# Optimization experiments

Hardware: AMD Instinct MI355X
Metric: run time of the kernel (lower is better)

Reference implementation:

```python
import jax, jax.numpy as jnp
import numpy as np

NMS_THRESH = 0.3  # default nms_thresh in DetNet.predict


def setup_inputs() -> dict:
    key = jax.random.key(0)
    k1, k2, k3, k4 = jax.random.split(key, 4)
    W, N = 8, 1024
    det = jax.random.uniform(k1, (W, N, 5), dtype=jnp.float32)          # (conf, cx, cy, w, h) in [0,1)
    offsets = jax.random.uniform(k2, (W, 5), dtype=jnp.float32) * 0.5   # window offset vector (0, left, top, 0, 0)-like
    scales = jax.random.uniform(k3, (W, 5), dtype=jnp.float32) * 0.5 + 0.25  # window scale vector
    b = jax.random.uniform(k4, (W, 4), dtype=jnp.float32)
    # (valid_left, valid_right, valid_top, valid_bottom) with left<right, top<bottom
    bounds = jnp.stack([0.3 * b[:, 0], 0.7 + 0.3 * b[:, 1],
                        0.3 * b[:, 2], 0.7 + 0.3 * b[:, 3]], axis=-1)
    return {"det": det, "offsets": offsets, "scales": scales, "bounds": bounds}


def _pairwise_iou(boxes):
    # boxes: [M,4] in (x1,y1,x2,y2)
    x1, y1, x2, y2 = boxes[:, 0], boxes[:, 1], boxes[:, 2], boxes[:, 3]
    area = jnp.clip(x2 - x1, 0.0) * jnp.clip(y2 - y1, 0.0)              # [M]
    iw = jnp.clip(jnp.minimum(x2[:, None], x2[None, :]) - jnp.maximum(x1[:, None], x1[None, :]), 0.0)
    ih = jnp.clip(jnp.minimum(y2[:, None], y2[None, :]) - jnp.maximum(y1[:, None], y1[None, :]), 0.0)
    inter = iw * ih                                                     # [M,M]
    union = area[:, None] + area[None, :] - inter
    return inter / jnp.maximum(union, 1e-9)


def reference(det, offsets, scales, bounds):
    W, N, _ = det.shape
    M = W * N
    cx, cy = det[..., 1], det[..., 2]                                    # [W,N]
    left, right = bounds[:, 0:1], bounds[:, 1:2]
    top, bottom = bounds[:, 2:3], bounds[:, 3:4]
    valid = (cx < right) & (cx > left) & (cy < bottom) & (cy > top)      # [W,N] border mask
    # torch.addcmul(offset, d, scale) = offset + d * scale
    d = (offsets[:, None, :] + det * scales[:, None, :]).reshape(M, 5)
    valid = valid.reshape(M)
    scores = jnp.where(valid, d[:, 0], -1.0)                             # invalid boxes never kept
    order = jnp.argsort(-scores)                                         # descending confidence
    d_s = d[order]                                                       # [M,5]
    s_s = scores[order]
    # point_form: (cx,cy,w,h) -> (x1,y1,x2,y2)
    cxy, wh = d_s[:, 1:3], d_s[:, 3:5]
    boxes = jnp.concatenate([cxy - wh * 0.5, cxy + wh * 0.5], axis=-1)
    iou = jax.lax.stop_gradient(_pairwise_iou(boxes))                    # [M,M], suppression is non-diff
    s_c = jax.lax.stop_gradient(s_s)
    idx = jnp.arange(M)

    def body(i, keep):
        # suppressed if any kept higher-score box overlaps > thresh
        sup = jnp.any(keep & (idx < i) & (iou[:, i] > NMS_THRESH))
        return keep.at[i].set(jnp.logical_and(~sup, s_c[i] > 0.0))

    keep = jax.lax.fori_loop(0, M, body, jnp.ones((M,), dtype=bool))
    return d_s * keep[:, None].astype(d_s.dtype)                         # [M,5], suppressed rows zeroed
```

## Files before the change

### kernel.cpp

```cpp
#include <hip/hip_runtime.h>
#include <cstdint>


#define M_TOT 8192
#define NMS_T 0.3f

#define WS_BOX   65536
#define WS_D     196608
#define WS_VCNT  360448
#define WS_ZROW  393216
#define WS_MASK  524288

typedef unsigned long long u64t;

__device__ __forceinline__ uint32_t desc_key(float sv) {
    uint32_t u = __float_as_uint(sv);
    uint32_t m = (u & 0x80000000u) ? ~u : (u | 0x80000000u);
    return ~m;
}

__device__ __forceinline__ u64t rdl64(u64t v, int sl) {
    unsigned lo = (unsigned)__builtin_amdgcn_readlane((int)(unsigned)v, sl);
    unsigned hi = (unsigned)__builtin_amdgcn_readlane((int)(unsigned)(v >> 32), sl);
    return ((u64t)hi << 32) | lo;
}
__device__ __forceinline__ u64t rdfl64(u64t v) {
    unsigned lo = (unsigned)__builtin_amdgcn_readfirstlane((int)(unsigned)v);
    unsigned hi = (unsigned)__builtin_amdgcn_readfirstlane((int)(unsigned)(v >> 32));
    return ((u64t)hi << 32) | lo;
}

__device__ __forceinline__ int scatter_one(
    int i, int rank, u64t key,
    const float* __restrict__ det, const float* __restrict__ offsets,
    const float* __restrict__ scales,
    float4* __restrict__ boxes_srt, float* __restrict__ d_srt)
{
    uint32_t dkey = (uint32_t)(key >> 16);
    if (dkey >= 0x7FFFFFFFu) return 0;
    int g = i >> 10;
    float d0 = __fadd_rn(offsets[g*5+0], __fmul_rn(det[i*5+0], scales[g*5+0]));
    float d1 = __fadd_rn(offsets[g*5+1], __fmul_rn(det[i*5+1], scales[g*5+1]));
    float d2 = __fadd_rn(offsets[g*5+2], __fmul_rn(det[i*5+2], scales[g*5+2]));
    float d3 = __fadd_rn(offsets[g*5+3], __fmul_rn(det[i*5+3], scales[g*5+3]));
    float d4 = __fadd_rn(offsets[g*5+4], __fmul_rn(det[i*5+4], scales[g*5+4]));
    d_srt[rank*5+0] = d0; d_srt[rank*5+1] = d1; d_srt[rank*5+2] = d2;
    d_srt[rank*5+3] = d3; d_srt[rank*5+4] = d4;
    float hw = __fmul_rn(d3, 0.5f), hh = __fmul_rn(d4, 0.5f);
    boxes_srt[rank] = make_float4(__fsub_rn(d1, hw), __fsub_rn(d2, hh),
                                  __fadd_rn(d1, hw), __fadd_rn(d2, hh));
    return 1;
}

__global__ __launch_bounds__(256) void k2_rank(
    const float* __restrict__ det, const float* __restrict__ offsets,
    const float* __restrict__ scales, const float* __restrict__ bounds,
    float4* __restrict__ boxes_srt, float* __restrict__ d_srt,
    unsigned int* __restrict__ vcnt, u64t* __restrict__ zrow,
    float* __restrict__ out)
{
    __shared__ u64t skey[M_TOT];
    __shared__ float soff[40], sscl[40], sbnd[32];
    __shared__ int sTop;
    int t = threadIdx.x;
    int lane = t & 63;
    if (t == 0) sTop = 0;
    if (t < 40) { soff[t] = offsets[t]; sscl[t] = scales[t]; }
    if (t < 32) { sbnd[t] = bounds[t]; }
    if (blockIdx.x == 0 && t < 128) zrow[t] = 0ull;
    __syncthreads();

    #pragma unroll 4
    for (int s = 0; s < 32; ++s) {
        int u = s * 256 + t;
        int g = u >> 10;
        float raw_s = det[u * 5 + 0];
        float cx    = det[u * 5 + 1];
        float cy    = det[u * 5 + 2];
        float score = __fadd_rn(soff[g * 5 + 0], __fmul_rn(raw_s, sscl[g * 5 + 0]));
        bool valid = (cx < sbnd[g*4+1]) && (cx > sbnd[g*4+0]) &&
                     (cy < sbnd[g*4+3]) && (cy > sbnd[g*4+2]);
        float sv = valid ? score : -1.0f;
        uint32_t dk = desc_key(sv);
        bool push = dk < 0x7FFFFFFFu;
        u64t key = ((u64t)dk << 16) | (unsigned)u;
        u64t bal = __ballot(push);
        if (bal) {
            int lw = 0;
            if (lane == 0) lw = atomicAdd(&sTop, __popcll(bal));
            int wbase = __builtin_amdgcn_readfirstlane(lw);
            if (push) {
                int off = __popcll(bal & ((1ull << lane) - 1ull));
                skey[wbase + off] = key;
            }
        }
    }
    __syncthreads();
    int V = sTop;
    int Vpad = (V + 15) & ~15;
    if (t < Vpad - V) skey[V + t] = ~0ull;
    {
        int zb = blockIdx.x * 160;
        for (int z = zb + t; z < zb + 160; z += 256) out[z] = 0.0f;
    }
    __syncthreads();
    if (t == 0) *vcnt = (unsigned)V;

    int grp = t >> 3;
    int jq  = t & 7;
    int i = blockIdx.x * 32 + grp;
    int g = i >> 10;
    float raw_s = det[i * 5 + 0];
    float cx    = det[i * 5 + 1];
    float cy    = det[i * 5 + 2];
    float score = __fadd_rn(soff[g * 5 + 0], __fmul_rn(raw_s, sscl[g * 5 + 0]));
    bool valid = (cx < sbnd[g*4+1]) && (cx > sbnd[g*4+0]) &&
                 (cy < sbnd[g*4+3]) && (cy > sbnd[g*4+2]);
    float sv = valid ? score : -1.0f;
    uint32_t dk = desc_key(sv);
    u64t ki = ((u64t)dk << 16) | (unsigned)i;
    const ulonglong2* skey2 = (const ulonglong2*)skey;
    int c = 0;
    int nit = Vpad >> 4;
    #pragma unroll 4
    for (int it = 0; it < nit; ++it) {
        ulonglong2 kj = skey2[it * 8 + jq];
        c += (kj.x < ki) + (kj.y < ki);
    }
    c += __shfl_xor(c, 1);
    c += __shfl_xor(c, 2);
    c += __shfl_xor(c, 4);
    if (jq == 0)
        scatter_one(i, c, ki, det, offsets, scales, boxes_srt, d_srt);
}

__global__ __launch_bounds__(256) void k_mask(
    const float4* __restrict__ boxes_srt,
    const unsigned int* __restrict__ vcnt,
    u64t* __restrict__ mask)
{
    __shared__ float4 sb[16 * 65];
    __shared__ float  sa[16 * 65];
    int V = (int)*vcnt;
    int bx = blockIdx.x, by = blockIdx.y;
    if (bx * 32 >= V) return;
    if (by * 1024 >= V) return;
    if (by * 16 + 15 < (bx * 32) >> 6) return;
    int nc = (V + 63) >> 6;
    int tid = threadIdx.x;
    int cbase = by * 1024;
    for (int u = tid; u < 1024; u += 256) {
        float4 b = boxes_srt[cbase + u];
        int c = u >> 6, jj = u & 63;
        sb[c * 65 + jj] = b;
        sa[c * 65 + jj] = __fmul_rn(fmaxf(__fsub_rn(b.z, b.x), 0.0f),
                                    fmaxf(__fsub_rn(b.w, b.y), 0.0f));
    }
    __syncthreads();
    int r = bx * 32 + (tid >> 3);
    if (r >= V) return;
    float4 bi = boxes_srt[r];
    float ai = __fmul_rn(fmaxf(__fsub_rn(bi.z, bi.x), 0.0f),
                         fmaxf(__fsub_rn(bi.w, bi.y), 0.0f));
    int rw = r >> 6;
    #pragma unroll
    for (int k = 0; k < 2; ++k) {
        int wl = (tid & 7) + k * 8;
        int w = by * 16 + wl;
        if (w < rw || w >= nc) continue;
        u64t bits = 0;
        #pragma unroll 4
        for (int jj = 0; jj < 64; ++jj) {
            float4 bj = sb[wl * 65 + jj];
            float aj = sa[wl * 65 + jj];
            float iw = fmaxf(__fsub_rn(fminf(bi.z, bj.z), fmaxf(bi.x, bj.x)), 0.0f);
            float ih = fmaxf(__fsub_rn(fminf(bi.w, bj.w), fmaxf(bi.y, bj.y)), 0.0f);
            float inter = __fmul_rn(iw, ih);
            float uni   = __fsub_rn(__fadd_rn(ai, aj), inter);
            float iou   = __fdiv_rn(inter, fmaxf(uni, 1e-9f));
            int j = w * 64 + jj;
            if (j > r && iou > NMS_T) bits |= 1ull << jj;
        }
        mask[(size_t)r * 128 + w] = bits;
    }
}

struct WSlot { ulonglong2 dl, dh, n1l, n1h, n2l, n2h; };

__device__ __forceinline__ void fill_words(
    const u64t* __restrict__ mask, int lane, int T, WSlot& w)
{
    int rl = min(T * 128 + lane,      M_TOT - 1);
    int rh = min(T * 128 + 64 + lane, M_TOT - 1);
    const ulonglong2* mrl = (const ulonglong2*)(mask + (size_t)rl * 128);
    const ulonglong2* mrh = (const ulonglong2*)(mask + (size_t)rh * 128);
    int p0 = min(T,     63);
    int p1 = min(T + 1, 63);
    int p2 = min(T + 2, 63);
    w.dl  = mrl[p0]; w.dh  = mrh[p0];
    w.n1l = mrl[p1]; w.n1h = mrh[p1];
    w.n2l = mrl[p2]; w.n2h = mrh[p2];
}

__device__ __forceinline__ void res_step(
    const u64t* __restrict__ mask,
    u64t* sdead, u64t* ck, volatile int* res_prog, volatile int* h_prog,
    int lane, int nc, int T,
    u64t& cA_lo, u64t& cA_hi, u64t& cB_lo, u64t& cB_hi, WSlot& w)
{
    if (T >= 3) {
        int need = T - 2;
        while (true) {
            int hp = (lane < 7) ? h_prog[lane] : 0x7FFFFFFF;
            if (__ballot(hp < need) == 0ull) break;
        }
    }
    u64t dlo = rdfl64(((volatile u64t*)sdead)[2 * T]);
    u64t dhi = rdfl64(((volatile u64t*)sdead)[2 * T + 1]);
    u64t live_lo = ~(dlo | cA_lo);
    u64t live_hi = ~(dhi | cA_hi);
    u64t km_lo = 0, km_hi = 0;
    while (live_lo) {
        int bs = (int)__builtin_ctzll(live_lo);
        km_lo |= 1ull << bs;
        u64t rml = rdl64(w.dl.x, bs);
        u64t rmh = rdl64(w.dl.y, bs);
        live_lo &= ~rml & ~(1ull << bs);
        live_hi &= ~rmh;
    }
    while (live_hi) {
        int bs = (int)__builtin_ctzll(live_hi);
        km_hi |= 1ull << bs;
        u64t rmh = rdl64(w.dh.y, bs);
        live_hi &= ~rmh & ~(1ull << bs);
    }
    if (lane == 0) { ck[2 * T] = km_lo; ck[2 * T + 1] = km_hi; }
    __threadfence_block();
    if (lane == 0) *res_prog = T + 1;
    u64t c1l = 0, c1h = 0, c2l = 0, c2h = 0;
    u64t km = km_lo;
    while (km) {
        int b = (int)__builtin_ctzll(km); km &= km - 1;
        c1l |= rdl64(w.n1l.x, b); c1h |= rdl64(w.n1l.y, b);
        c2l |= rdl64(w.n2l.x, b); c2h |= rdl64(w.n2l.y, b);
    }
    km = km_hi;
    while (km) {
        int b = (int)__builtin_ctzll(km); km &= km - 1;
        c1l |= rdl64(w.n1h.x, b); c1h |= rdl64(w.n1h.y, b);
        c2l |= rdl64(w.n2h.x, b); c2h |= rdl64(w.n2h.y, b);
    }
    cA_lo = cB_lo | c1l; cA_hi = cB_hi | c1h;
    cB_lo = c2l;         cB_hi = c2h;
    fill_words(mask, lane, T + 3, w);
}

__global__ __launch_bounds__(512) void k3_serial(
    const u64t* __restrict__ mask, const u64t* __restrict__ zrow,
    const float* __restrict__ d_srt, const unsigned int* __restrict__ vcnt,
    float* __restrict__ out)
{
    __shared__ u64t sdead[128];
    __shared__ u64t ck[128];
    __shared__ int  res_prog;
    __shared__ int  h_prog[7];
    int tid = threadIdx.x, wv = tid >> 6, lane = tid & 63;
    int V = (int)*vcnt;
    int nc = (V + 127) >> 7;
    if (tid < 128) {
        int bw = tid * 64;
        u64t w0 = 0;
        if (bw >= V)           w0 = ~0ull;
        else if (bw + 64 > V)  w0 = (~0ull) << (V - bw);
        sdead[tid] = w0;
        ck[tid] = 0ull;
    }
    if (tid == 0) res_prog = 0;
    if (tid < 7)  h_prog[tid] = tid;
    __syncthreads();

    if (wv == 0) {
        u64t cA_lo = 0, cA_hi = 0, cB_lo = 0, cB_hi = 0;
        WSlot WA, WB, WC;
        fill_words(mask, lane, 0, WA);
        fill_words(mask, lane, 1, WB);
        fill_words(mask, lane, 2, WC);
        for (int t = 0; t < nc; t += 3) {
            res_step(mask, sdead, ck, &res_prog, h_prog, lane, nc, t,
                     cA_lo, cA_hi, cB_lo, cB_hi, WA);
            if (t + 1 < nc)
                res_step(mask, sdead, ck, &res_prog, h_prog, lane, nc, t + 1,
                         cA_lo, cA_hi, cB_lo, cB_hi, WB);
            if (t + 2 < nc)
                res_step(mask, sdead, ck, &res_prog, h_prog, lane, nc, t + 2,
                         cA_lo, cA_hi, cB_lo, cB_hi, WC);
        }
    } else {
        int hh = wv - 1;
        for (int c = hh; c < nc; c += 7) {
            while (*(volatile int*)&res_prog <= c) __builtin_amdgcn_s_sleep(1);
            u64t kl = ((volatile u64t*)ck)[2 * c];
            u64t kh = ((volatile u64t*)ck)[2 * c + 1];
            if (kl | kh) {
                int base = c * 128;
                u64t ax = 0, ay = 0;
                while (kl | kh) {
                    ulonglong2 b[4];
                    #pragma unroll
                    for (int q = 0; q < 4; ++q) {
                        const ulonglong2* ptr;
                        if (kl) {
                            int b_ = __builtin_ctzll(kl); kl &= kl - 1;
                            ptr = (const ulonglong2*)(mask + (size_t)(base + b_) * 128) + lane;
                        } else if (kh) {
                            int b_ = __builtin_ctzll(kh); kh &= kh - 1;
                            ptr = (const ulonglong2*)(mask + (size_t)(base + 64 + b_) * 128) + lane;
                        } else {
                            ptr = (const ulonglong2*)zrow + lane;
                        }
                        b[q] = *ptr;
                    }
                    ax |= b[0].x | b[1].x | b[2].x | b[3].x;
                    ay |= b[0].y | b[1].y | b[2].y | b[3].y;
                }
                atomicOr(&sdead[2 * lane],     ax);
                atomicOr(&sdead[2 * lane + 1], ay);
            }
            __threadfence_block();
            if (lane == 0) ((volatile int*)h_prog)[hh] = c + 7;
        }
        if (lane == 0) ((volatile int*)h_prog)[hh] = 0x7FFFFFFF;
    }
    __syncthreads();
    if (tid < 128) {
        u64t m = ck[tid];
        while (m) {
            int b = __builtin_ctzll(m); m &= m - 1;
            int rr = tid * 64 + b;
            out[rr * 5 + 0] = d_srt[rr * 5 + 0];
            out[rr * 5 + 1] = d_srt[rr * 5 + 1];
            out[rr * 5 + 2] = d_srt[rr * 5 + 2];
            out[rr * 5 + 3] = d_srt[rr * 5 + 3];
            out[rr * 5 + 4] = d_srt[rr * 5 + 4];
        }
    }
}

extern "C" void kernel_launch(void* const* d_in, const int* in_sizes, int n_in,
                              void* d_out, int out_size, void* d_ws, size_t ws_size,
                              hipStream_t stream) {
    const float* det     = (const float*)d_in[0];
    const float* offsets = (const float*)d_in[1];
    const float* scales  = (const float*)d_in[2];
    const float* bounds  = (const float*)d_in[3];
    float* out = (float*)d_out;
    char* ws = (char*)d_ws;
    float4*       boxes = (float4*)(ws + WS_BOX);
    float*        d_srt = (float*)(ws + WS_D);
    unsigned int* vcnt  = (unsigned int*)(ws + WS_VCNT);
    u64t*         zrow  = (u64t*)(ws + WS_ZROW);
    u64t*         mask  = (u64t*)(ws + WS_MASK);

    k2_rank<<<256, 256, 0, stream>>>(det, offsets, scales, bounds, boxes, d_srt, vcnt, zrow, out);
    k_mask<<<dim3(256, 8), 256, 0, stream>>>(boxes, vcnt, mask);
    k3_serial<<<1, 512, 0, stream>>>(mask, zrow, d_srt, vcnt, out);
}
```

Baseline: 157.0 us.

## Preload diagonal mask band into LDS and shorten serial resolver lookahead

The serial NMS resolver wave no longer register-prefetches three chunks of mask words from global memory. Instead, all 512 threads first copy the diagonal band (current and next chunk words) of the first 24 chunks into shared memory. The resolver then carries one chunk of lookahead instead of two and waits on helper progress of T-1. Chunks beyond the band still load directly from global memory. The aim is to take global load latency off the serial critical path, at the cost of an upfront bulk copy and about 96KB of LDS. The smaller lookahead also ties the resolver more tightly to the helper waves.

```diff
diff --git a/kernel.cpp b/kernel.cpp
--- a/kernel.cpp
+++ b/kernel.cpp
@@ -4,6 +4,7 @@
 
 #define M_TOT 8192
 #define NMS_T 0.3f
+#define PCMAX 24
 
 #define WS_BOX   65536
 #define WS_D     196608
@@ -18,7 +19,6 @@
     uint32_t m = (u & 0x80000000u) ? ~u : (u | 0x80000000u);
     return ~m;
 }
-
 __device__ __forceinline__ u64t rdl64(u64t v, int sl) {
     unsigned lo = (unsigned)__builtin_amdgcn_readlane((int)(unsigned)v, sl);
     unsigned hi = (unsigned)__builtin_amdgcn_readlane((int)(unsigned)(v >> 32), sl);
@@ -30,14 +30,14 @@
     return ((u64t)hi << 32) | lo;
 }
 
-__device__ __forceinline__ int scatter_one(
+__device__ __forceinline__ void scatter_one(
     int i, int rank, u64t key,
     const float* __restrict__ det, const float* __restrict__ offsets,
     const float* __restrict__ scales,
     float4* __restrict__ boxes_srt, float* __restrict__ d_srt)
 {
     uint32_t dkey = (uint32_t)(key >> 16);
-    if (dkey >= 0x7FFFFFFFu) return 0;
+    if (dkey >= 0x7FFFFFFFu) return;
     int g = i >> 10;
     float d0 = __fadd_rn(offsets[g*5+0], __fmul_rn(det[i*5+0], scales[g*5+0]));
     float d1 = __fadd_rn(offsets[g*5+1], __fmul_rn(det[i*5+1], scales[g*5+1]));
@@ -49,7 +49,6 @@
     float hw = __fmul_rn(d3, 0.5f), hh = __fmul_rn(d4, 0.5f);
     boxes_srt[rank] = make_float4(__fsub_rn(d1, hw), __fsub_rn(d2, hh),
                                   __fadd_rn(d1, hw), __fadd_rn(d2, hh));
-    return 1;
 }
 
 __global__ __launch_bounds__(256) void k2_rank(
@@ -185,81 +184,12 @@
     }
 }
 
-struct WSlot { ulonglong2 dl, dh, n1l, n1h, n2l, n2h; };
-
-__device__ __forceinline__ void fill_words(
-    const u64t* __restrict__ mask, int lane, int T, WSlot& w)
-{
-    int rl = min(T * 128 + lane,      M_TOT - 1);
-    int rh = min(T * 128 + 64 + lane, M_TOT - 1);
-    const ulonglong2* mrl = (const ulonglong2*)(mask + (size_t)rl * 128);
-    const ulonglong2* mrh = (const ulonglong2*)(mask + (size_t)rh * 128);
-    int p0 = min(T,     63);
-    int p1 = min(T + 1, 63);
-    int p2 = min(T + 2, 63);
-    w.dl  = mrl[p0]; w.dh  = mrh[p0];
-    w.n1l = mrl[p1]; w.n1h = mrh[p1];
-    w.n2l = mrl[p2]; w.n2h = mrh[p2];
-}
-
-__device__ __forceinline__ void res_step(
-    const u64t* __restrict__ mask,
-    u64t* sdead, u64t* ck, volatile int* res_prog, volatile int* h_prog,
-    int lane, int nc, int T,
-    u64t& cA_lo, u64t& cA_hi, u64t& cB_lo, u64t& cB_hi, WSlot& w)
-{
-    if (T >= 3) {
-        int need = T - 2;
-        while (true) {
-            int hp = (lane < 7) ? h_prog[lane] : 0x7FFFFFFF;
-            if (__ballot(hp < need) == 0ull) break;
-        }
-    }
-    u64t dlo = rdfl64(((volatile u64t*)sdead)[2 * T]);
-    u64t dhi = rdfl64(((volatile u64t*)sdead)[2 * T + 1]);
-    u64t live_lo = ~(dlo | cA_lo);
-    u64t live_hi = ~(dhi | cA_hi);
-    u64t km_lo = 0, km_hi = 0;
-    while (live_lo) {
-        int bs = (int)__builtin_ctzll(live_lo);
-        km_lo |= 1ull << bs;
-        u64t rml = rdl64(w.dl.x, bs);
-        u64t rmh = rdl64(w.dl.y, bs);
-        live_lo &= ~rml & ~(1ull << bs);
-        live_hi &= ~rmh;
-    }
-    while (live_hi) {
-        int bs = (int)__builtin_ctzll(live_hi);
-        km_hi |= 1ull << bs;
-        u64t rmh = rdl64(w.dh.y, bs);
-        live_hi &= ~rmh & ~(1ull << bs);
-    }
-    if (lane == 0) { ck[2 * T] = km_lo; ck[2 * T + 1] = km_hi; }
-    __threadfence_block();
-    if (lane == 0) *res_prog = T + 1;
-    u64t c1l = 0, c1h = 0, c2l = 0, c2h = 0;
-    u64t km = km_lo;
-    while (km) {
-        int b = (int)__builtin_ctzll(km); km &= km - 1;
-        c1l |= rdl64(w.n1l.x, b); c1h |= rdl64(w.n1l.y, b);
-        c2l |= rdl64(w.n2l.x, b); c2h |= rdl64(w.n2l.y, b);
-    }
-    km = km_hi;
-    while (km) {
-        int b = (int)__builtin_ctzll(km); km &= km - 1;
-        c1l |= rdl64(w.n1h.x, b); c1h |= rdl64(w.n1h.y, b);
-        c2l |= rdl64(w.n2h.x, b); c2h |= rdl64(w.n2h.y, b);
-    }
-    cA_lo = cB_lo | c1l; cA_hi = cB_hi | c1h;
-    cB_lo = c2l;         cB_hi = c2h;
-    fill_words(mask, lane, T + 3, w);
-}
-
 __global__ __launch_bounds__(512) void k3_serial(
     const u64t* __restrict__ mask, const u64t* __restrict__ zrow,
     const float* __restrict__ d_srt, const unsigned int* __restrict__ vcnt,
     float* __restrict__ out)
 {
+    __shared__ u64t sband[PCMAX * 128 * 4];
     __shared__ u64t sdead[128];
     __shared__ u64t ck[128];
     __shared__ int  res_prog;
@@ -267,6 +197,8 @@
     int tid = threadIdx.x, wv = tid >> 6, lane = tid & 63;
     int V = (int)*vcnt;
     int nc = (V + 127) >> 7;
+    int PC = min(nc, PCMAX);
+
     if (tid < 128) {
         int bw = tid * 64;
         u64t w0 = 0;
@@ -277,23 +209,82 @@
     }
     if (tid == 0) res_prog = 0;
     if (tid < 7)  h_prog[tid] = tid;
+    for (int e = tid; e < PC * 128; e += 512) {
+        int c = e >> 7;
+        const u64t* rp = mask + (size_t)e * 128;
+        ulonglong2 lo = *(const ulonglong2*)(rp + 2 * c);
+        ulonglong2 hi = *(const ulonglong2*)(rp + 2 * c + 2);
+        ulonglong2* bp = (ulonglong2*)(sband + (size_t)e * 4);
+        bp[0] = lo; bp[1] = hi;
+    }
     __syncthreads();
 
     if (wv == 0) {
-        u64t cA_lo = 0, cA_hi = 0, cB_lo = 0, cB_hi = 0;
-        WSlot WA, WB, WC;
-        fill_words(mask, lane, 0, WA);
-        fill_words(mask, lane, 1, WB);
-        fill_words(mask, lane, 2, WC);
-        for (int t = 0; t < nc; t += 3) {
-            res_step(mask, sdead, ck, &res_prog, h_prog, lane, nc, t,
-                     cA_lo, cA_hi, cB_lo, cB_hi, WA);
-            if (t + 1 < nc)
-                res_step(mask, sdead, ck, &res_prog, h_prog, lane, nc, t + 1,
-                         cA_lo, cA_hi, cB_lo, cB_hi, WB);
-            if (t + 2 < nc)
-                res_step(mask, sdead, ck, &res_prog, h_prog, lane, nc, t + 2,
-                         cA_lo, cA_hi, cB_lo, cB_hi, WC);
+        u64t cA_lo = 0, cA_hi = 0;
+        for (int T = 0; T < nc; ++T) {
+            ulonglong2 bl, bln, bh, bhn;
+            if (T < PC) {
+                const ulonglong2* p0 = (const ulonglong2*)(sband + (size_t)(T * 128 + lane) * 4);
+                const ulonglong2* p1 = (const ulonglong2*)(sband + (size_t)(T * 128 + 64 + lane) * 4);
+                bl = p0[0]; bln = p0[1];
+                bh = p1[0]; bhn = p1[1];
+            } else {
+                int rl = min(T * 128 + lane,      M_TOT - 1);
+                int rh = min(T * 128 + 64 + lane, M_TOT - 1);
+                int w = min(2 * T, 124);
+                const u64t* rpl = mask + (size_t)rl * 128;
+                const u64t* rph = mask + (size_t)rh * 128;
+                bl  = *(const ulonglong2*)(rpl + w);
+                bln = *(const ulonglong2*)(rpl + w + 2);
+                bh  = *(const ulonglong2*)(rph + w);
+                bhn = *(const ulonglong2*)(rph + w + 2);
+            }
+            if (T >= 2) {
+                int need = T - 1;
+                while (true) {
+                    int hp = (lane < 7) ? ((volatile int*)h_prog)[lane] : 0x7FFFFFFF;
+                    if (__ballot(hp < need) == 0ull) break;
+                }
+            }
+            u64t dlo = rdfl64(((volatile u64t*)sdead)[2 * T]);
+            u64t dhi = rdfl64(((volatile u64t*)sdead)[2 * T + 1]);
+            u64t live_lo = ~(dlo | cA_lo);
+            u64t live_hi = ~(dhi | cA_hi);
+            int rem = V - T * 128;
+            if (rem < 128) {
+                live_lo &= (rem >= 64) ? ~0ull : ((rem <= 0) ? 0ull : ((1ull << rem) - 1ull));
+                int rh = rem - 64;
+                live_hi &= (rh >= 64) ? ~0ull : ((rh <= 0) ? 0ull : ((1ull << rh) - 1ull));
+            }
+            u64t km_lo = 0, km_hi = 0;
+            while (live_lo) {
+                int bs = (int)__builtin_ctzll(live_lo);
+                km_lo |= 1ull << bs;
+                u64t rml = rdl64(bl.x, bs);
+                u64t rmh = rdl64(bl.y, bs);
+                live_lo &= ~rml & ~(1ull << bs);
+                live_hi &= ~rmh;
+            }
+            while (live_hi) {
+                int bs = (int)__builtin_ctzll(live_hi);
+                km_hi |= 1ull << bs;
+                u64t rmh = rdl64(bh.y, bs);
+                live_hi &= ~rmh & ~(1ull << bs);
+            }
+            if (lane == 0) { ck[2 * T] = km_lo; ck[2 * T + 1] = km_hi; }
+            __threadfence_block();
+            if (lane == 0) *(volatile int*)&res_prog = T + 1;
+            u64t c1l = 0, c1h = 0, km = km_lo;
+            while (km) {
+                int b = (int)__builtin_ctzll(km); km &= km - 1;
+                c1l |= rdl64(bln.x, b); c1h |= rdl64(bln.y, b);
+            }
+            km = km_hi;
+            while (km) {
+                int b = (int)__builtin_ctzll(km); km &= km - 1;
+                c1l |= rdl64(bhn.x, b); c1h |= rdl64(bhn.y, b);
+            }
+            cA_lo = c1l; cA_hi = c1h;
         }
     } else {
         int hh = wv - 1;
```

After: 148.4 us. 5.5% less time.
